# Performance work log

Measured on AMD Instinct MI355X. Metric: run time of the kernel, lower is better.

The kernel has to match this reference:

```python
import jax, jax.numpy as jnp
import numpy as np

NUM_HEADS = 8
LN_EPS = 1e-5


def setup_inputs() -> dict:
    key = jax.random.key(0)
    ks = jax.random.split(key, 9)
    B, C, H, W = 8, 512, 32, 32
    s = 1.0 / np.sqrt(C)
    return {
        "f_curr": jax.random.normal(ks[0], (B, C, H, W), dtype=jnp.float32),
        "f_prev": jax.random.normal(ks[1], (B, C, H, W), dtype=jnp.float32),
        "f_next": jax.random.normal(ks[2], (B, C, H, W), dtype=jnp.float32),
        "Wq": jax.random.normal(ks[3], (C, C), dtype=jnp.float32) * s,
        "Wk": jax.random.normal(ks[4], (C, C), dtype=jnp.float32) * s,
        "Wv": jax.random.normal(ks[5], (C, C), dtype=jnp.float32) * s,
        "Wo": jax.random.normal(ks[6], (C, C), dtype=jnp.float32) * s,
        "gamma": jnp.ones((C,), dtype=jnp.float32),
        "beta": jnp.zeros((C,), dtype=jnp.float32),
    }


def _flatten(f):
    # [B,C,H,W] -> [B, H*W, C]
    B, C, H, W = f.shape
    return f.reshape(B, C, H * W).transpose(0, 2, 1)


def reference(f_curr, f_prev, f_next, Wq, Wk, Wv, Wo, gamma, beta):
    B, C, H, W = f_curr.shape
    N = H * W
    hd = C // NUM_HEADS
    scale = hd ** -0.5

    curr_flat = _flatten(f_curr)                              # [B,N,C]
    neigh_flat = jnp.concatenate([_flatten(f_prev), _flatten(f_next)], axis=1)  # [B,2N,C]

    # torch Linear (no bias): y = x @ W.T
    Q = curr_flat @ Wq.T                                      # [B,N,C]
    K = neigh_flat @ Wk.T                                     # [B,2N,C]
    V = neigh_flat @ Wv.T                                     # [B,2N,C]

    def split_heads(t, L):
        return t.reshape(B, L, NUM_HEADS, hd).transpose(0, 2, 1, 3)  # [B,h,L,hd]

    Qh = split_heads(Q, N)
    Kh = split_heads(K, 2 * N)
    Vh = split_heads(V, 2 * N)

    scores = jnp.einsum("bhnd,bhmd->bhnm", Qh, Kh) * scale    # [B,h,N,2N]
    attn = jax.nn.softmax(scores, axis=-1)
    out = jnp.einsum("bhnm,bhmd->bhnd", attn, Vh)             # [B,h,N,hd]

    out = out.transpose(0, 2, 1, 3).reshape(B, N, C)          # merge heads
    out = curr_flat + out @ Wo.T                              # residual

    # LayerNorm over channel dim
    mu = jnp.mean(out, axis=-1, keepdims=True)
    var = jnp.mean(jnp.square(out - mu), axis=-1, keepdims=True)
    out = (out - mu) * jax.lax.rsqrt(var + LN_EPS) * gamma + beta

    return out.transpose(0, 2, 1).reshape(B, C, H, W)
```

## Files before the change

### kernel.cpp

```cpp
#include <hip/hip_runtime.h>
#include <hip/hip_bf16.h>
#include <math.h>

#define NH 8
#define HD 64
#define CH 512
#define NT 1024
#define NB 8

typedef __bf16 bf16_t;
typedef bf16_t bf16x8 __attribute__((ext_vector_type(8)));
typedef bf16_t bf16x4 __attribute__((ext_vector_type(4)));
typedef float  f32x4  __attribute__((ext_vector_type(4)));
typedef float  f32x16 __attribute__((ext_vector_type(16)));
typedef unsigned u32x4 __attribute__((ext_vector_type(4)));

#define MFMA16(a, b, c) __builtin_amdgcn_mfma_f32_16x16x32_bf16((a), (b), (c), 0, 0, 0)
#define MFMA32(a, b, c) __builtin_amdgcn_mfma_f32_32x32x16_bf16((a), (b), (c), 0, 0, 0)

__device__ __forceinline__ void gload16(const void* g, void* l) {
    __builtin_amdgcn_global_load_lds(
        (const __attribute__((address_space(1))) void*)g,
        (__attribute__((address_space(3))) void*)l, 16, 0, 0);
}

__device__ __forceinline__ unsigned cvtpk(float lo, float hi) {
    unsigned r;
    asm("v_cvt_pk_bf16_f32 %0, %1, %2" : "=v"(r) : "v"(lo), "v"(hi));
    return r;
}

__device__ __forceinline__ void plswap(unsigned& a, unsigned& b) {
    asm("v_permlane32_swap_b32 %0, %1" : "+v"(a), "+v"(b));
}

__global__ __launch_bounds__(256) void prep_kernel(
    const float* __restrict__ fc, const float* __restrict__ fp,
    const float* __restrict__ fn, bf16_t* __restrict__ Xc,
    bf16_t* __restrict__ Xn)
{
    __shared__ __align__(16) bf16_t tile[64 * 64];
    const int t = threadIdx.x;
    const int y = blockIdx.y;
    const int b = y / 3, ft = y % 3;
    const int c0 = (blockIdx.x & 7) * 64;
    const int n0 = (blockIdx.x >> 3) * 64;

    const float* src; bf16_t* dst;
    if (ft == 0)      { src = fc + (size_t)b * CH * NT; dst = Xc + (size_t)b * NT * CH; }
    else if (ft == 1) { src = fp + (size_t)b * CH * NT; dst = Xn + (size_t)b * 2 * NT * CH; }
    else              { src = fn + (size_t)b * CH * NT; dst = Xn + (size_t)b * 2 * NT * CH + (size_t)NT * CH; }

    const int nb = t & 15, cb = t >> 4;
    float4 ld[4];
#pragma unroll
    for (int i = 0; i < 4; ++i)
        ld[i] = *(const float4*)(src + (size_t)(c0 + cb * 4 + i) * NT + n0 + nb * 4);
    const float* lf = (const float*)ld;
#pragma unroll
    for (int j = 0; j < 4; ++j) {
        int n = nb * 4 + j;
        int v = (n >> 2) & 14;
        bf16x4 wv = { (bf16_t)lf[0 * 4 + j], (bf16_t)lf[1 * 4 + j],
                      (bf16_t)lf[2 * 4 + j], (bf16_t)lf[3 * 4 + j] };
        *(bf16x4*)(tile + n * 64 + ((cb ^ v) * 4)) = wv;
    }
    __syncthreads();
#pragma unroll
    for (int i = 0; i < 2; ++i) {
        int gid = t + i * 256;
        int n = gid >> 3, c16 = gid & 7;
        int v = (n >> 2) & 14;
        bf16x8 val = *(const bf16x8*)(tile + n * 64 + (((2 * c16) ^ v) * 4));
        *(bf16x8*)(dst + (size_t)(n0 + n) * CH + c0 + c16 * 8) = val;
    }
}

__global__ __launch_bounds__(256) void wcvt_kernel(
    const float* __restrict__ Wq, const float* __restrict__ Wk,
    const float* __restrict__ Wv, const float* __restrict__ Wo,
    bf16_t* __restrict__ Wb)
{
    const int m = blockIdx.y;
    const float* src = (m == 0) ? Wq : (m == 1) ? Wk : (m == 2) ? Wv : Wo;
    bf16_t* dst = Wb + (size_t)m * CH * CH;
    int gid = blockIdx.x * 256 + threadIdx.x;
    float4 v = *(const float4*)(src + (size_t)gid * 4);
    bf16x4 o = { (bf16_t)v.x, (bf16_t)v.y, (bf16_t)v.z, (bf16_t)v.w };
    *(bf16x4*)(dst + (size_t)gid * 4) = o;
}

template <bool SWAP>
__device__ __forceinline__ void gemm_core(const bf16_t* __restrict__ A,
                                          const bf16_t* __restrict__ B,
                                          bf16_t* aT, bf16_t* bT,
                                          f32x4 acc[4][4])
{
    const int t = threadIdx.x, w = t >> 6, lane = t & 63;
    const int lid = lane & 15, quad = lane >> 4;
    const int wm = w >> 1, wn = w & 1;
    const int l4 = lane >> 2, k4 = lane & 3;

    for (int kt = 0; kt < 16; ++kt) {
        const int k0 = kt * 32;
        __syncthreads();
#pragma unroll
        for (int i = 0; i < 2; ++i) {
            int q = w * 2 + i;
            int row = q * 16 + l4;
            int kk = k4 ^ ((row >> 1) & 3);
            gload16(A + (size_t)row * CH + k0 + kk * 8, aT + q * 512);
            gload16(B + (size_t)row * CH + k0 + kk * 8, bT + q * 512);
        }
        __syncthreads();

        const bf16_t* mT = SWAP ? bT : aT;
        const bf16_t* nT = SWAP ? aT : bT;
        bf16x8 mf[4], nf[4];
#pragma unroll
        for (int i = 0; i < 4; ++i) {
            int row = wm * 64 + i * 16 + lid;
            int kw = quad ^ ((row >> 1) & 3);
            mf[i] = *(const bf16x8*)(mT + row * 32 + kw * 8);
        }
#pragma unroll
        for (int i = 0; i < 4; ++i) {
            int row = wn * 64 + i * 16 + lid;
            int kw = quad ^ ((row >> 1) & 3);
            nf[i] = *(const bf16x8*)(nT + row * 32 + kw * 8);
        }
#pragma unroll
        for (int mi = 0; mi < 4; ++mi)
#pragma unroll
            for (int ni = 0; ni < 4; ++ni)
                acc[mi][ni] = MFMA16(mf[mi], nf[ni], acc[mi][ni]);
    }
}

__global__ __launch_bounds__(256) void qkv_kernel(
    const bf16_t* __restrict__ Xc, const bf16_t* __restrict__ Xn,
    const bf16_t* __restrict__ Wb,
    bf16_t* __restrict__ Qn, bf16_t* __restrict__ Kn, bf16_t* __restrict__ Vt)
{
    __shared__ __align__(16) bf16_t aT[128 * 32];
    __shared__ __align__(16) bf16_t bT[128 * 32];
    const int bx = blockIdx.x, b = blockIdx.y;
    const int t = threadIdx.x, w = t >> 6, lane = t & 63;
    const int lid = lane & 15, quad = lane >> 4;
    const int wm = w >> 1, wn = w & 1;
    const float QSC = 0.125f * 1.44269504f;

    f32x4 acc[4][4] = {};

    if (bx < 96) {
        const bf16_t* A; const bf16_t* B; bf16_t* O; float scale;
        if (bx < 32) {
            int nt = bx >> 2, ct = bx & 3;
            A = Xc + (size_t)b * NT * CH + (size_t)nt * 128 * CH;
            B = Wb + (size_t)0 * CH * CH + (size_t)ct * 128 * CH;
            O = Qn + (size_t)b * NT * CH + (size_t)nt * 128 * CH + ct * 128;
            scale = QSC;
        } else {
            int j = bx - 32, nt = j >> 2, ct = j & 3;
            A = Xn + (size_t)b * 2 * NT * CH + (size_t)nt * 128 * CH;
            B = Wb + (size_t)1 * CH * CH + (size_t)ct * 128 * CH;
            O = Kn + (size_t)b * 2 * NT * CH + (size_t)nt * 128 * CH + ct * 128;
            scale = 1.0f;
        }
        gemm_core<false>(A, B, aT, bT, acc);
#pragma unroll
        for (int mi = 0; mi < 4; ++mi)
#pragma unroll
            for (int ni = 0; ni < 4; ++ni)
#pragma unroll
                for (int r = 0; r < 4; ++r) {
                    int n  = wm * 64 + mi * 16 + quad * 4 + r;
                    int co = wn * 64 + ni * 16 + lid;
                    O[(size_t)n * CH + co] = (bf16_t)(acc[mi][ni][r] * scale);
                }
    } else {
        int j = bx - 96, nt = j >> 2, ct = j & 3;
        const bf16_t* A = Xn + (size_t)b * 2 * NT * CH + (size_t)nt * 128 * CH;
        const bf16_t* B = Wb + (size_t)2 * CH * CH + (size_t)ct * 128 * CH;
        bf16_t* O = Vt + (size_t)b * CH * 2 * NT + (size_t)ct * 128 * 2 * NT + nt * 128;
        gemm_core<true>(A, B, aT, bT, acc);
#pragma unroll
        for (int mi = 0; mi < 4; ++mi)
#pragma unroll
            for (int ni = 0; ni < 4; ++ni)
#pragma unroll
                for (int r = 0; r < 4; ++r) {
                    int co_l  = wm * 64 + mi * 16 + quad * 4 + r;
                    int key_l = wn * 64 + ni * 16 + lid;
                    O[(size_t)co_l * (2 * NT) + key_l] = (bf16_t)acc[mi][ni][r];
                }
    }
}

__global__ __launch_bounds__(256, 2) void attn_kernel(
    const bf16_t* __restrict__ Qn, const bf16_t* __restrict__ Kn,
    const bf16_t* __restrict__ Vt, bf16_t* __restrict__ AOn)
{
    __shared__ __align__(16) char smem[72192];
    bf16_t* const kbuf0 = (bf16_t*)smem;
    bf16_t* const kbuf1 = (bf16_t*)(smem + 18432);
    bf16_t* const vbuf0 = (bf16_t*)(smem + 36864);
    bf16_t* const vbuf1 = (bf16_t*)(smem + 54272);
    float*  const l_scr = (float*)(smem + 71680);

    const int t = threadIdx.x;
    const int w = t >> 6, lane = t & 63;
    const int wq = w >> 1, wk = w & 1;
    const int l31 = lane & 31, h = lane >> 5;

    const int bid = blockIdx.x;
    const int xcd = bid & 7, ii = bid >> 3;
    const int grp = xcd * 8 + (ii >> 3);
    const int qt  = ii & 7;
    const int b = grp >> 3, hh = grp & 7;
    const int q0 = qt * 128;

    const bf16_t* Qb  = Qn + ((size_t)b * NT + q0) * CH + hh * HD;
    const bf16_t* Kb  = Kn + (size_t)b * 2 * NT * CH + hh * HD;
    const bf16_t* Vtb = Vt + ((size_t)b * CH + hh * HD) * (2 * NT);
    bf16_t* AOb = AOn + ((size_t)b * NT + q0) * CH + hh * HD;

    bf16x8 kreg[4], vreg[4];
#pragma unroll
    for (int i = 0; i < 4; ++i) {
        int gid = t + i * 256;
        int qr = gid >> 3, c8 = (gid & 7) * 8;
        *(bf16x8*)(kbuf1 + qr * 72 + (c8 ^ (qr & 24))) =
            *(const bf16x8*)(Qb + (size_t)qr * CH + c8);
    }
#pragma unroll
    for (int i = 0; i < 4; ++i) {
        int gid = t + i * 256;
        int kr = gid >> 3, c8 = (gid & 7) * 8;
        kreg[i] = *(const bf16x8*)(Kb + (size_t)kr * CH + c8);
        int dr = gid >> 4, c16 = (gid & 15) * 8;
        vreg[i] = *(const bf16x8*)(Vtb + (size_t)dr * (2 * NT) + c16);
    }
#pragma unroll
    for (int i = 0; i < 4; ++i) {
        int gid = t + i * 256;
        int kr = gid >> 3, c8 = (gid & 7) * 8;
        *(bf16x8*)(kbuf0 + kr * 72 + (c8 ^ (kr & 24))) = kreg[i];
        int dr = gid >> 4, c16 = (gid & 15) * 8;
        *(bf16x8*)(vbuf0 + dr * 136 + (c16 ^ (dr & 24))) = vreg[i];
    }
    __syncthreads();

    bf16x8 qf[2][4];
#pragma unroll
    for (int nf = 0; nf < 2; ++nf)
#pragma unroll
        for (int ks = 0; ks < 4; ++ks) {
            int row = wq * 64 + nf * 32 + l31;
            int col = (ks * 16 + h * 8) ^ (row & 24);
            qf[nf][ks] = *(const bf16x8*)(kbuf1 + row * 72 + col);
        }
#pragma unroll
    for (int i = 0; i < 4; ++i) {
        int gid = t + i * 256;
        int kr = gid >> 3, c8 = (gid & 7) * 8;
        kreg[i] = *(const bf16x8*)(Kb + (size_t)(128 + kr) * CH + c8);
        int dr = gid >> 4, c16 = (gid & 15) * 8;
        vreg[i] = *(const bf16x8*)(Vtb + (size_t)dr * (2 * NT) + 128 + c16);
    }
    __syncthreads();

    f32x16 o[2][2] = {};
    float lpart[2] = {0.f, 0.f};

    for (int kt = 0; kt < 16; ++kt) {
        const int cur = kt & 1;
        bf16_t* const kb_w = cur ? kbuf0 : kbuf1;
        bf16_t* const vb_w = cur ? vbuf0 : vbuf1;
        const bf16_t* const kb_r = cur ? kbuf1 : kbuf0;
        const bf16_t* const vb_r = cur ? vbuf1 : vbuf0;

#pragma unroll
        for (int i = 0; i < 4; ++i) {
            int gid = t + i * 256;
            int kr = gid >> 3, c8 = (gid & 7) * 8;
            *(bf16x8*)(kb_w + kr * 72 + (c8 ^ (kr & 24))) = kreg[i];
            int dr = gid >> 4, c16 = (gid & 15) * 8;
            *(bf16x8*)(vb_w + dr * 136 + (c16 ^ (dr & 24))) = vreg[i];
        }
        {
            const int pfb = (kt + 2 < 16) ? (kt + 2) * 128 : 0;
#pragma unroll
            for (int i = 0; i < 4; ++i) {
                int gid = t + i * 256;
                int kr = gid >> 3, c8 = (gid & 7) * 8;
                kreg[i] = *(const bf16x8*)(Kb + (size_t)(pfb + kr) * CH + c8);
                int dr = gid >> 4, c16 = (gid & 15) * 8;
                vreg[i] = *(const bf16x8*)(Vtb + (size_t)dr * (2 * NT) + pfb + c16);
            }
        }

        f32x16 s[2][2] = {};
        __builtin_amdgcn_s_setprio(1);
#pragma unroll
        for (int ks = 0; ks < 4; ++ks) {
            bf16x8 af[2];
#pragma unroll
            for (int mf = 0; mf < 2; ++mf) {
                int arow = wk * 64 + mf * 32 + l31;
                int acol = (ks * 16 + h * 8) ^ (arow & 24);
                af[mf] = *(const bf16x8*)(kb_r + arow * 72 + acol);
            }
#pragma unroll
            for (int mf = 0; mf < 2; ++mf)
#pragma unroll
                for (int nf = 0; nf < 2; ++nf)
                    s[mf][nf] = MFMA32(af[mf], qf[nf][ks], s[mf][nf]);
        }
        __builtin_amdgcn_s_setprio(0);

#pragma unroll
        for (int mf = 0; mf < 2; ++mf) {
            bf16x8 pfrag[2][2];
#pragma unroll
            for (int nf = 0; nf < 2; ++nf) {
                float p[16];
#pragma unroll
                for (int r = 0; r < 16; ++r) p[r] = exp2f(s[mf][nf][r]);
                lpart[nf] += ((p[0] + p[1]) + (p[2] + p[3]))
                           + ((p[4] + p[5]) + (p[6] + p[7]))
                           + ((p[8] + p[9]) + (p[10] + p[11]))
                           + ((p[12] + p[13]) + (p[14] + p[15]));
                unsigned a0 = cvtpk(p[0], p[1]),   b0 = cvtpk(p[4], p[5]);
                unsigned a1 = cvtpk(p[2], p[3]),   b1 = cvtpk(p[6], p[7]);
                unsigned a2 = cvtpk(p[8], p[9]),   b2 = cvtpk(p[12], p[13]);
                unsigned a3 = cvtpk(p[10], p[11]), b3 = cvtpk(p[14], p[15]);
                plswap(a0, b0); plswap(a1, b1); plswap(a2, b2); plswap(a3, b3);
                u32x4 f0 = { a0, a1, b0, b1 };
                u32x4 f1 = { a2, a3, b2, b3 };
                pfrag[nf][0] = __builtin_bit_cast(bf16x8, f0);
                pfrag[nf][1] = __builtin_bit_cast(bf16x8, f1);
            }
            __builtin_amdgcn_s_setprio(1);
#pragma unroll
            for (int fi = 0; fi < 2; ++fi) {
                const int ks = mf * 2 + fi;
                bf16x8 av[2];
#pragma unroll
                for (int df = 0; df < 2; ++df) {
                    int vrow = df * 32 + l31;
                    int vcol = (wk * 64 + ks * 16 + h * 8) ^ (vrow & 24);
                    av[df] = *(const bf16x8*)(vb_r + vrow * 136 + vcol);
                }
#pragma unroll
                for (int df = 0; df < 2; ++df)
#pragma unroll
                    for (int nf = 0; nf < 2; ++nf)
                        o[df][nf] = MFMA32(av[df], pfrag[nf][fi], o[df][nf]);
            }
            __builtin_amdgcn_s_setprio(0);
        }
        __syncthreads();
    }

    float l2[2];
#pragma unroll
    for (int nf = 0; nf < 2; ++nf)
        l2[nf] = lpart[nf] + __shfl_xor(lpart[nf], 32);

    float* const scr_all = (float*)smem;
    bf16_t* const obuf = (bf16_t*)(smem + 36864);

    if (wk == 1) {
        float* scr = scr_all + wq * 4352;
#pragma unroll
        for (int df = 0; df < 2; ++df)
#pragma unroll
            for (int nf = 0; nf < 2; ++nf) {
                int qrow = nf * 32 + l31;
#pragma unroll
                for (int g = 0; g < 4; ++g) {
                    int d = df * 32 + 8 * g + 4 * h;
                    f32x4 v = { o[df][nf][4 * g + 0], o[df][nf][4 * g + 1],
                                o[df][nf][4 * g + 2], o[df][nf][4 * g + 3] };
                    *(f32x4*)(scr + qrow * 68 + d) = v;
                }
            }
        if (h == 0) {
            l_scr[wq * 64 + 0 * 32 + l31] = l2[0];
            l_scr[wq * 64 + 1 * 32 + l31] = l2[1];
        }
    }
    __syncthreads();

    if (wk == 0) {
        const float* scr = scr_all + wq * 4352;
        float inv[2];
#pragma unroll
        for (int nf = 0; nf < 2; ++nf)
            inv[nf] = 1.0f / (l2[nf] + l_scr[wq * 64 + nf * 32 + l31]);
#pragma unroll
        for (int df = 0; df < 2; ++df)
#pragma unroll
            for (int nf = 0; nf < 2; ++nf) {
                int qrow = nf * 32 + l31;
#pragma unroll
                for (int g = 0; g < 4; ++g) {
                    int d = df * 32 + 8 * g + 4 * h;
                    f32x4 part = *(const f32x4*)(scr + qrow * 68 + d);
                    bf16x4 ov = {
                        (bf16_t)((o[df][nf][4 * g + 0] + part.x) * inv[nf]),
                        (bf16_t)((o[df][nf][4 * g + 1] + part.y) * inv[nf]),
                        (bf16_t)((o[df][nf][4 * g + 2] + part.z) * inv[nf]),
                        (bf16_t)((o[df][nf][4 * g + 3] + part.w) * inv[nf]) };
                    int qg = wq * 64 + qrow;
                    *(bf16x4*)(obuf + qg * 72 + (d ^ (qg & 24))) = ov;
                }
            }
    }
    __syncthreads();

#pragma unroll
    for (int i = 0; i < 4; ++i) {
        int gid = t + i * 256;
        int qr = gid >> 3, c8 = (gid & 7) * 8;
        *(bf16x8*)(AOb + (size_t)qr * CH + c8) =
            *(const bf16x8*)(obuf + qr * 72 + (c8 ^ (qr & 24)));
    }
}

__global__ __launch_bounds__(256) void proj_kernel(
    const bf16_t* __restrict__ AOn, const bf16_t* __restrict__ Wb,
    const float* __restrict__ fc, float* __restrict__ Zt)
{
    __shared__ __align__(16) bf16_t aT[128 * 32];
    __shared__ __align__(16) bf16_t bT[128 * 32];
    const int bx = blockIdx.x, b = blockIdx.y;
    const int nt = bx >> 2, ct = bx & 3;
    const int t = threadIdx.x, w = t >> 6, lane = t & 63;
    const int lid = lane & 15, quad = lane >> 4;
    const int wm = w >> 1, wn = w & 1;

    const bf16_t* A = AOn + (size_t)b * NT * CH + (size_t)nt * 128 * CH;
    const bf16_t* B = Wb + (size_t)3 * CH * CH + (size_t)ct * 128 * CH;

    f32x4 acc[4][4] = {};
    gemm_core<true>(A, B, aT, bT, acc);

    const size_t bofs = (size_t)b * CH * NT;
#pragma unroll
    for (int mi = 0; mi < 4; ++mi)
#pragma unroll
        for (int ni = 0; ni < 4; ++ni)
#pragma unroll
            for (int r = 0; r < 4; ++r) {
                int co_l = wm * 64 + mi * 16 + quad * 4 + r;
                int n_l  = wn * 64 + ni * 16 + lid;
                size_t idx = bofs + (size_t)(ct * 128 + co_l) * NT + nt * 128 + n_l;
                Zt[idx] = acc[mi][ni][r] + fc[idx];
            }
}

__global__ __launch_bounds__(256) void stats_kernel(
    const float* __restrict__ Zt, float* __restrict__ mu_buf,
    float* __restrict__ rs_buf)
{
    __shared__ float sS[1024], sQ[1024];
    const int b = blockIdx.y, n0 = blockIdx.x * 64;
    const int t = threadIdx.x, w = t >> 6, lane = t & 63;
    const int co_off = lane >> 4, n4 = lane & 15;
    const float* Zb = Zt + (size_t)b * CH * NT + n0 + n4 * 4;

    f32x4 s = {0, 0, 0, 0}, q = {0, 0, 0, 0};
    for (int it = 0; it < 32; ++it) {
        int co = w * 4 + co_off + it * 16;
        f32x4 z = *(const f32x4*)(Zb + (size_t)co * NT);
#pragma unroll
        for (int c = 0; c < 4; ++c) { s[c] += z[c]; q[c] += z[c] * z[c]; }
    }
#pragma unroll
    for (int c = 0; c < 4; ++c) { sS[t * 4 + c] = s[c]; sQ[t * 4 + c] = q[c]; }
    __syncthreads();

    if (t < 64) {
        int n4r = t >> 2, comp = t & 3;
        float ss = 0.f, qq = 0.f;
#pragma unroll
        for (int i = 0; i < 16; ++i) {
            int idx = ((i >> 2) * 64 + (i & 3) * 16 + n4r) * 4 + comp;
            ss += sS[idx]; qq += sQ[idx];
        }
        float mu  = ss * (1.0f / 512.0f);
        float var = qq * (1.0f / 512.0f) - mu * mu;
        mu_buf[(size_t)b * NT + n0 + t] = mu;
        rs_buf[(size_t)b * NT + n0 + t] = rsqrtf(var + 1e-5f);
    }
}

__global__ __launch_bounds__(256) void apply_kernel(
    const float* __restrict__ Zt, const float* __restrict__ mu_buf,
    const float* __restrict__ rs_buf, const float* __restrict__ gamma,
    const float* __restrict__ beta, float* __restrict__ out)
{
    const int row = blockIdx.x;
    const int co = row & 511, b = row >> 9;
    const int t = threadIdx.x;
    const float g = gamma[co], be = beta[co];
    const size_t base = (size_t)row * NT + t * 4;
    f32x4 z  = *(const f32x4*)(Zt + base);
    f32x4 mu = *(const f32x4*)(mu_buf + (size_t)b * NT + t * 4);
    f32x4 rs = *(const f32x4*)(rs_buf + (size_t)b * NT + t * 4);
    f32x4 o;
#pragma unroll
    for (int c = 0; c < 4; ++c) o[c] = (z[c] - mu[c]) * rs[c] * g + be;
    *(f32x4*)(out + base) = o;
}

extern "C" void kernel_launch(void* const* d_in, const int* in_sizes, int n_in,
                              void* d_out, int out_size, void* d_ws, size_t ws_size,
                              hipStream_t stream)
{
    (void)in_sizes; (void)n_in; (void)out_size; (void)ws_size;
    const float* fc    = (const float*)d_in[0];
    const float* fp    = (const float*)d_in[1];
    const float* fn    = (const float*)d_in[2];
    const float* Wq    = (const float*)d_in[3];
    const float* Wk    = (const float*)d_in[4];
    const float* Wv    = (const float*)d_in[5];
    const float* Wo    = (const float*)d_in[6];
    const float* gamma = (const float*)d_in[7];
    const float* beta  = (const float*)d_in[8];
    float* out = (float*)d_out;

    char* ws = (char*)d_ws;
    bf16_t* Xn  = (bf16_t*)(ws);
    bf16_t* Qn  = (bf16_t*)(ws + 16777216);
    bf16_t* Kn  = (bf16_t*)(ws + 25165824);
    bf16_t* Xc  = (bf16_t*)(ws + 41943040);
    bf16_t* AOn = Xc;
    bf16_t* Vt  = (bf16_t*)(ws + 50331648);
    bf16_t* Wb  = (bf16_t*)(ws + 67108864);
    float*  mu  = (float*)(ws + 69206016);
    float*  rs  = (float*)(ws + 69238784);
    float*  Zt  = (float*)(ws);

    prep_kernel<<<dim3(128, 24), 256, 0, stream>>>(fc, fp, fn, Xc, Xn);
    wcvt_kernel<<<dim3(256, 4), 256, 0, stream>>>(Wq, Wk, Wv, Wo, Wb);
    qkv_kernel<<<dim3(160, 8), 256, 0, stream>>>(Xc, Xn, Wb, Qn, Kn, Vt);
    attn_kernel<<<dim3(512), 256, 0, stream>>>(Qn, Kn, Vt, AOn);
    proj_kernel<<<dim3(32, 8), 256, 0, stream>>>(AOn, Wb, fc, Zt);
    stats_kernel<<<dim3(16, 8), 256, 0, stream>>>(Zt, mu, rs);
    apply_kernel<<<4096, 256, 0, stream>>>(Zt, mu, rs, gamma, beta, out);
}
```

Baseline: 239.9 us.

## Load attention K/V fragments directly from global and fuse LN stats into projection

The attention kernel drops its LDS double-buffered K/V staging and its per-tile barriers, loading MFMA fragments straight from global memory (relying on L2 reuse), and switches to the hardware exp2 builtin. The LayerNorm statistics kernel is removed: the projection epilogue accumulates per-token sum and sum-of-squares via shuffles, LDS and atomics into buffers zeroed by the weight-convert kernel, and the apply kernel computes mean and rstd inline. This cuts one launch and a full read of Zt, but the attention loads become uncoalesced global reads with no barrier-synchronised prefetch, and the atomic float accumulation makes the stats non-deterministic.

```diff
diff --git a/kernel.cpp b/kernel.cpp
--- a/kernel.cpp
+++ b/kernel.cpp
@@ -17,6 +17,7 @@
 
 #define MFMA16(a, b, c) __builtin_amdgcn_mfma_f32_16x16x32_bf16((a), (b), (c), 0, 0, 0)
 #define MFMA32(a, b, c) __builtin_amdgcn_mfma_f32_32x32x16_bf16((a), (b), (c), 0, 0, 0)
+#define EXP2(x) __builtin_amdgcn_exp2f(x)
 
 __device__ __forceinline__ void gload16(const void* g, void* l) {
     __builtin_amdgcn_global_load_lds(
@@ -79,7 +80,7 @@
 __global__ __launch_bounds__(256) void wcvt_kernel(
     const float* __restrict__ Wq, const float* __restrict__ Wk,
     const float* __restrict__ Wv, const float* __restrict__ Wo,
-    bf16_t* __restrict__ Wb)
+    bf16_t* __restrict__ Wb, float* __restrict__ SQz)
 {
     const int m = blockIdx.y;
     const float* src = (m == 0) ? Wq : (m == 1) ? Wk : (m == 2) ? Wv : Wo;
@@ -88,6 +89,10 @@
     float4 v = *(const float4*)(src + (size_t)gid * 4);
     bf16x4 o = { (bf16_t)v.x, (bf16_t)v.y, (bf16_t)v.z, (bf16_t)v.w };
     *(bf16x4*)(dst + (size_t)gid * 4) = o;
+    if (m == 0 && blockIdx.x < 16) {
+        f32x4 zz = {0.f, 0.f, 0.f, 0.f};
+        *(f32x4*)(SQz + (size_t)(blockIdx.x * 256 + threadIdx.x) * 4) = zz;
+    }
 }
 
 template <bool SWAP>
@@ -201,12 +206,10 @@
     const bf16_t* __restrict__ Qn, const bf16_t* __restrict__ Kn,
     const bf16_t* __restrict__ Vt, bf16_t* __restrict__ AOn)
 {
-    __shared__ __align__(16) char smem[72192];
-    bf16_t* const kbuf0 = (bf16_t*)smem;
-    bf16_t* const kbuf1 = (bf16_t*)(smem + 18432);
-    bf16_t* const vbuf0 = (bf16_t*)(smem + 36864);
-    bf16_t* const vbuf1 = (bf16_t*)(smem + 54272);
-    float*  const l_scr = (float*)(smem + 71680);
+    __shared__ __align__(16) char smem[55808];
+    float*  const scr_all = (float*)smem;
+    bf16_t* const obuf    = (bf16_t*)(smem + 36864);
+    float*  const l_scr   = (float*)(smem + 55296);
 
     const int t = threadIdx.x;
     const int w = t >> 6, lane = t & 63;
@@ -225,99 +228,47 @@
     const bf16_t* Vtb = Vt + ((size_t)b * CH + hh * HD) * (2 * NT);
     bf16_t* AOb = AOn + ((size_t)b * NT + q0) * CH + hh * HD;
 
-    bf16x8 kreg[4], vreg[4];
-#pragma unroll
-    for (int i = 0; i < 4; ++i) {
-        int gid = t + i * 256;
-        int qr = gid >> 3, c8 = (gid & 7) * 8;
-        *(bf16x8*)(kbuf1 + qr * 72 + (c8 ^ (qr & 24))) =
-            *(const bf16x8*)(Qb + (size_t)qr * CH + c8);
-    }
-#pragma unroll
-    for (int i = 0; i < 4; ++i) {
-        int gid = t + i * 256;
-        int kr = gid >> 3, c8 = (gid & 7) * 8;
-        kreg[i] = *(const bf16x8*)(Kb + (size_t)kr * CH + c8);
-        int dr = gid >> 4, c16 = (gid & 15) * 8;
-        vreg[i] = *(const bf16x8*)(Vtb + (size_t)dr * (2 * NT) + c16);
-    }
-#pragma unroll
-    for (int i = 0; i < 4; ++i) {
-        int gid = t + i * 256;
-        int kr = gid >> 3, c8 = (gid & 7) * 8;
-        *(bf16x8*)(kbuf0 + kr * 72 + (c8 ^ (kr & 24))) = kreg[i];
-        int dr = gid >> 4, c16 = (gid & 15) * 8;
-        *(bf16x8*)(vbuf0 + dr * 136 + (c16 ^ (dr & 24))) = vreg[i];
-    }
-    __syncthreads();
+    const bf16_t* Qrow = Qb  + (size_t)(wq * 64 + l31) * CH + h * 8;
+    const bf16_t* Krow = Kb  + (size_t)(wk * 64 + l31) * CH + h * 8;
+    const bf16_t* Vrow = Vtb + (size_t)l31 * (2 * NT) + wk * 64 + h * 8;
 
     bf16x8 qf[2][4];
 #pragma unroll
     for (int nf = 0; nf < 2; ++nf)
 #pragma unroll
-        for (int ks = 0; ks < 4; ++ks) {
-            int row = wq * 64 + nf * 32 + l31;
-            int col = (ks * 16 + h * 8) ^ (row & 24);
-            qf[nf][ks] = *(const bf16x8*)(kbuf1 + row * 72 + col);
-        }
-#pragma unroll
-    for (int i = 0; i < 4; ++i) {
-        int gid = t + i * 256;
-        int kr = gid >> 3, c8 = (gid & 7) * 8;
-        kreg[i] = *(const bf16x8*)(Kb + (size_t)(128 + kr) * CH + c8);
-        int dr = gid >> 4, c16 = (gid & 15) * 8;
-        vreg[i] = *(const bf16x8*)(Vtb + (size_t)dr * (2 * NT) + 128 + c16);
-    }
-    __syncthreads();
+        for (int ks = 0; ks < 4; ++ks)
+            qf[nf][ks] = *(const bf16x8*)(Qrow + (size_t)nf * 32 * CH + ks * 16);
 
     f32x16 o[2][2] = {};
     float lpart[2] = {0.f, 0.f};
 
     for (int kt = 0; kt < 16; ++kt) {
-        const int cur = kt & 1;
-        bf16_t* const kb_w = cur ? kbuf0 : kbuf1;
-        bf16_t* const vb_w = cur ? vbuf0 : vbuf1;
-        const bf16_t* const kb_r = cur ? kbuf1 : kbuf0;
-        const bf16_t* const vb_r = cur ? vbuf1 : vbuf0;
-
-#pragma unroll
-        for (int i = 0; i < 4; ++i) {
-            int gid = t + i * 256;
-            int kr = gid >> 3, c8 = (gid & 7) * 8;
-            *(bf16x8*)(kb_w + kr * 72 + (c8 ^ (kr & 24))) = kreg[i];
-            int dr = gid >> 4, c16 = (gid & 15) * 8;
-            *(bf16x8*)(vb_w + dr * 136 + (c16 ^ (dr & 24))) = vreg[i];
-        }
-        {
-            const int pfb = (kt + 2 < 16) ? (kt + 2) * 128 : 0;
-#pragma unroll
-            for (int i = 0; i < 4; ++i) {
-                int gid = t + i * 256;
-                int kr = gid >> 3, c8 = (gid & 7) * 8;
-                kreg[i] = *(const bf16x8*)(Kb + (size_t)(pfb + kr) * CH + c8);
-                int dr = gid >> 4, c16 = (gid & 15) * 8;
-                vreg[i] = *(const bf16x8*)(Vtb + (size_t)dr * (2 * NT) + pfb + c16);
-            }
-        }
+        const size_t kb = (size_t)kt * 128;
+
+        bf16x8 kf[2][4];
+#pragma unroll
+        for (int mf = 0; mf < 2; ++mf)
+#pragma unroll
+            for (int ks = 0; ks < 4; ++ks)
+                kf[mf][ks] = *(const bf16x8*)(Krow + (kb + mf * 32) * CH + ks * 16);
 
         f32x16 s[2][2] = {};
         __builtin_amdgcn_s_setprio(1);
 #pragma unroll
-        for (int ks = 0; ks < 4; ++ks) {
-            bf16x8 af[2];
-#pragma unroll
-            for (int mf = 0; mf < 2; ++mf) {
-                int arow = wk * 64 + mf * 32 + l31;
-                int acol = (ks * 16 + h * 8) ^ (arow & 24);
-                af[mf] = *(const bf16x8*)(kb_r + arow * 72 + acol);
-            }
+        for (int ks = 0; ks < 4; ++ks)
 #pragma unroll
             for (int mf = 0; mf < 2; ++mf)
 #pragma unroll
                 for (int nf = 0; nf < 2; ++nf)
-                    s[mf][nf] = MFMA32(af[mf], qf[nf][ks], s[mf][nf]);
-        }
+                    s[mf][nf] = MFMA32(kf[mf][ks], qf[nf][ks], s[mf][nf]);
         __builtin_amdgcn_s_setprio(0);
+
+        bf16x8 vf[2][4];
+#pragma unroll
+        for (int df = 0; df < 2; ++df)
+#pragma unroll
+            for (int ks = 0; ks < 4; ++ks)
+                vf[df][ks] = *(const bf16x8*)(Vrow + (size_t)df * 32 * (2 * NT) + kb + ks * 16);
 
 #pragma unroll
         for (int mf = 0; mf < 2; ++mf) {
@@ -326,7 +277,7 @@
             for (int nf = 0; nf < 2; ++nf) {
                 float p[16];
 #pragma unroll
-                for (int r = 0; r < 16; ++r) p[r] = exp2f(s[mf][nf][r]);
+                for (int r = 0; r < 16; ++r) p[r] = EXP2(s[mf][nf][r]);
                 lpart[nf] += ((p[0] + p[1]) + (p[2] + p[3]))
                            + ((p[4] + p[5]) + (p[6] + p[7]))
                            + ((p[8] + p[9]) + (p[10] + p[11]))
@@ -345,31 +296,20 @@
 #pragma unroll
             for (int fi = 0; fi < 2; ++fi) {
                 const int ks = mf * 2 + fi;
-                bf16x8 av[2];
-#pragma unroll
-                for (int df = 0; df < 2; ++df) {
-                    int vrow = df * 32 + l31;
-                    int vcol = (wk * 64 + ks * 16 + h * 8) ^ (vrow & 24);
-                    av[df] = *(const bf16x8*)(vb_r + vrow * 136 + vcol);
-                }
 #pragma unroll
                 for (int df = 0; df < 2; ++df)
 #pragma unroll
                     for (int nf = 0; nf < 2; ++nf)
-                        o[df][nf] = MFMA32(av[df], pfrag[nf][fi], o[df][nf]);
+                        o[df][nf] = MFMA32(vf[df][ks], pfrag[nf][fi], o[df][nf]);
             }
             __builtin_amdgcn_s_setprio(0);
         }
-        __syncthreads();
     }
 
     float l2[2];
 #pragma unroll
     for (int nf = 0; nf < 2; ++nf)
         l2[nf] = lpart[nf] + __shfl_xor(lpart[nf], 32);
-
-    float* const scr_all = (float*)smem;
-    bf16_t* const obuf = (bf16_t*)(smem + 36864);
 
     if (wk == 1) {
         float* scr = scr_all + wq * 4352;
@@ -431,7 +371,8 @@
 
 __global__ __launch_bounds__(256) void proj_kernel(
     const bf16_t* __restrict__ AOn, const bf16_t* __restrict__ Wb,
-    const float* __restrict__ fc, float* __restrict__ Zt)
+    const float* __restrict__ fc, float* __restrict__ Zt,
+    float* __restrict__ Ssum, float* __restrict__ Ssq)
 {
     __shared__ __align__(16) bf16_t aT[128 * 32];
     __shared__ __align__(16) bf16_t bT[128 * 32];
@@ -448,6 +389,7 @@
     gemm_core<true>(A, B, aT, bT, acc);
 
     const size_t bofs = (size_t)b * CH * NT;
+    float sP[4] = {0.f, 0.f, 0.f, 0.f}, qP[4] = {0.f, 0.f, 0.f, 0.f};
 #pragma unroll
     for (int mi = 0; mi < 4; ++mi)
 #pragma unroll
@@ -457,49 +399,38 @@
                 int co_l = wm * 64 + mi * 16 + quad * 4 + r;
                 int n_l  = wn * 64 + ni * 16 + lid;
                 size_t idx = bofs + (size_t)(ct * 128 + co_l) * NT + nt * 128 + n_l;
-                Zt[idx] = acc[mi][ni][r] + fc[idx];
+                float z = acc[mi][ni][r] + fc[idx];
+                Zt[idx] = z;
+                sP[ni] += z;
+                qP[ni] += z * z;
             }
-}
-
-__global__ __launch_bounds__(256) void stats_kernel(
-    const float* __restrict__ Zt, float* __restrict__ mu_buf,
-    float* __restrict__ rs_buf)
-{
-    __shared__ float sS[1024], sQ[1024];
-    const int b = blockIdx.y, n0 = blockIdx.x * 64;
-    const int t = threadIdx.x, w = t >> 6, lane = t & 63;
-    const int co_off = lane >> 4, n4 = lane & 15;
-    const float* Zb = Zt + (size_t)b * CH * NT + n0 + n4 * 4;
-
-    f32x4 s = {0, 0, 0, 0}, q = {0, 0, 0, 0};
-    for (int it = 0; it < 32; ++it) {
-        int co = w * 4 + co_off + it * 16;
-        f32x4 z = *(const f32x4*)(Zb + (size_t)co * NT);
-#pragma unroll
-        for (int c = 0; c < 4; ++c) { s[c] += z[c]; q[c] += z[c] * z[c]; }
-    }
-#pragma unroll
-    for (int c = 0; c < 4; ++c) { sS[t * 4 + c] = s[c]; sQ[t * 4 + c] = q[c]; }
+#pragma unroll
+    for (int ni = 0; ni < 4; ++ni) {
+        sP[ni] += __shfl_xor(sP[ni], 16);  sP[ni] += __shfl_xor(sP[ni], 32);
+        qP[ni] += __shfl_xor(qP[ni], 16);  qP[ni] += __shfl_xor(qP[ni], 32);
+    }
     __syncthreads();
-
-    if (t < 64) {
-        int n4r = t >> 2, comp = t & 3;
-        float ss = 0.f, qq = 0.f;
-#pragma unroll
-        for (int i = 0; i < 16; ++i) {
-            int idx = ((i >> 2) * 64 + (i & 3) * 16 + n4r) * 4 + comp;
-            ss += sS[idx]; qq += sQ[idx];
-        }
-        float mu  = ss * (1.0f / 512.0f);
-        float var = qq * (1.0f / 512.0f) - mu * mu;
-        mu_buf[(size_t)b * NT + n0 + t] = mu;
-        rs_buf[(size_t)b * NT + n0 + t] = rsqrtf(var + 1e-5f);
+    float* sRed = (float*)aT;
+    float* qRed = sRed + 256;
+    if (quad == 0) {
+#pragma unroll
+        for (int ni = 0; ni < 4; ++ni) {
+            sRed[w * 64 + ni * 16 + lid] = sP[ni];
+            qRed[w * 64 + ni * 16 + lid] = qP[ni];
+        }
+    }
+    __syncthreads();
+    if (t < 128) {
+        float s = sRed[t] + sRed[128 + t];
+        float q = qRed[t] + qRed[128 + t];
+        atomicAdd(&Ssum[(size_t)b * NT + nt * 128 + t], s);
+        atomicAdd(&Ssq [(size_t)b * NT + nt * 128 + t], q);
     }
 }
 
 __global__ __launch_bounds__(256) void apply_kernel(
-    const float* __restrict__ Zt, const float* __restrict__ mu_buf,
-    const float* __restrict__ rs_buf, const float* __restrict__ gamma,
+    const float* __restrict__ Zt, const float* __restrict__ Ssum,
+    const float* __restrict__ Ssq, const float* __restrict__ gamma,
     const float* __restrict__ beta, float* __restrict__ out)
 {
     const int row = blockIdx.x;
@@ -508,11 +439,16 @@
     const float g = gamma[co], be = beta[co];
     const size_t base = (size_t)row * NT + t * 4;
     f32x4 z  = *(const f32x4*)(Zt + base);
-    f32x4 mu = *(const f32x4*)(mu_buf + (size_t)b * NT + t * 4);
-    f32x4 rs = *(const f32x4*)(rs_buf + (size_t)b * NT + t * 4);
+    f32x4 S  = *(const f32x4*)(Ssum + (size_t)b * NT + t * 4);
+    f32x4 Q2 = *(const f32x4*)(Ssq  + (size_t)b * NT + t * 4);
     f32x4 o;
 #pragma unroll
-    for (int c = 0; c < 4; ++c) o[c] = (z[c] - mu[c]) * rs[c] * g + be;
+    for (int c = 0; c < 4; ++c) {
+        float mu  = S[c] * (1.0f / 512.0f);
+        float var = Q2[c] * (1.0f / 512.0f) - mu * mu;
+        float rs  = rsqrtf(var + 1e-5f);
+        o[c] = (z[c] - mu) * rs * g + be;
+    }
     *(f32x4*)(out + base) = o;
 }
 
@@ -540,15 +476,14 @@
     bf16_t* AOn = Xc;
     bf16_t* Vt  = (bf16_t*)(ws + 50331648);
     bf16_t* Wb  = (bf16_t*)(ws + 67108864);
-    float*  mu  = (float*)(ws + 69206016);
-    float*  rs  = (float*)(ws + 69238784);
+    float*  Ssum = (float*)(ws + 69206016);
+    float*  Ssq  = (float*)(ws + 69238784);
     float*  Zt  = (float*)(ws);
 
     prep_kernel<<<dim3(128, 24), 256, 0, stream>>>(fc, fp, fn, Xc, Xn);
-    wcvt_kernel<<<dim3(256, 4), 256, 0, stream>>>(Wq, Wk, Wv, Wo, Wb);
+    wcvt_kernel<<<dim3(256, 4), 256, 0, stream>>>(Wq, Wk, Wv, Wo, Wb, Ssum);
     qkv_kernel<<<dim3(160, 8), 256, 0, stream>>>(Xc, Xn, Wb, Qn, Kn, Vt);
     attn_kernel<<<dim3(512), 256, 0, stream>>>(Qn, Kn, Vt, AOn);
-    proj_kernel<<<dim3(32, 8), 256, 0, stream>>>(AOn, Wb, fc, Zt);
-    stats_kernel<<<dim3(16, 8), 256, 0, stream>>>(Zt, mu, rs);
-    apply_kernel<<<4096, 256, 0, stream>>>(Zt, mu, rs, gamma, beta, out);
-}
+    proj_kernel<<<dim3(32, 8), 256, 0, stream>>>(AOn, Wb, fc, Zt, Ssum, Ssq);
+    apply_kernel<<<4096, 256, 0, stream>>>(Zt, Ssum, Ssq, gamma, beta, out);
+}
```

After: 230.6 us. 1.04x faster.
